# Kernel tuning notes

Measured on AMD Instinct MI355X. Metric: run time of the kernel, lower is better.

The kernel has to match this reference:

```python
import jax, jax.numpy as jnp
import numpy as np


def setup_inputs() -> dict:
    key = jax.random.key(0)
    k1, k2 = jax.random.split(key)
    x = jax.random.normal(k1, (32, 64, 64, 64), dtype=jnp.float32)  # [B, C, H, W]
    limit = 3 ** 0.5
    embeddings = jax.random.uniform(k2, (64, 512), dtype=jnp.float32,
                                    minval=-limit, maxval=limit)  # [D, K]
    return {"x": x, "embeddings": embeddings}


def reference(x, embeddings):
    B, D, H, W = x.shape
    # NCHW -> NHWC -> [N, D]
    flat_x = jnp.transpose(x, (0, 2, 3, 1)).reshape(-1, D)
    distances = (
        jnp.sum(flat_x ** 2, axis=1, keepdims=True)
        - 2.0 * flat_x @ embeddings
        + jnp.sum(embeddings ** 2, axis=0, keepdims=True)
    )
    encoding_indices = jnp.argmin(distances, axis=1)  # [N]
    # gather codebook rows: embeddings.T is [K, D]
    quantized = embeddings.T[encoding_indices].reshape(B, H, W, D)
    quantized = jnp.transpose(quantized, (0, 3, 1, 2))  # back to NCHW
    commitment_loss = jnp.mean((x - jax.lax.stop_gradient(quantized)) ** 2)
    # straight-through estimator
    quantized_ste = x + jax.lax.stop_gradient(quantized - x)
    return quantized_ste, commitment_loss, encoding_indices.reshape(B, -1)
```

## Files before the change

kernel.cpp:

```cpp
#include <hip/hip_runtime.h>

#define D      64
#define K      512
#define Q_OFF  0
#define L_OFF  8388608
#define I_OFF  8388609

#define WS_ET    0
#define WS_EN    32768
#define WS_ENH   33280
#define WS_PART  33792

#define B_LO_OFF 4096

#define SEL_SCALE 16384.0f
#define SEL_BIAS  (160.0f * 16384.0f)

typedef __attribute__((ext_vector_type(8))) short short8;
typedef __attribute__((ext_vector_type(4))) float f32x4;

static __device__ __forceinline__ unsigned short f2bf(float f) {
    unsigned u = __float_as_uint(f);
    u += 0x7fffu + ((u >> 16) & 1u);
    return (unsigned short)(u >> 16);
}
static __device__ __forceinline__ float bf2f(unsigned short h) {
    return __uint_as_float(((unsigned)h) << 16);
}

__global__ __launch_bounds__(256) void vq_prep(const float* __restrict__ E,
                                               float* __restrict__ ws,
                                               float* __restrict__ out) {
    int g = blockIdx.x * 256 + threadIdx.x;
    int t = g >> 6, lane = g & 63;
    int col = lane & 15, kg = lane >> 4;
    int code = t * 16 + col;
    short8* bhp = (short8*)out;
    short8* blp = (short8*)out + B_LO_OFF;
#pragma unroll
    for (int s = 0; s < 2; ++s) {
        short8 h, l;
#pragma unroll
        for (int j = 0; j < 8; ++j) {
            int k = s * 32 + kg * 8 + j;
            float v = -E[k * K + code];
            unsigned short hb = f2bf(v);
            h[j] = (short)hb;
            l[j] = (short)f2bf(v - bf2f(hb));
        }
        bhp[(t * 2 + s) * 64 + lane] = h;
        blp[(t * 2 + s) * 64 + lane] = l;
    }
    if (g < K) {
        float nsq = 0.f;
#pragma unroll 8
        for (int d = 0; d < D; ++d) {
            float v = E[d * K + g];
            ws[WS_ET + g * D + d] = v;
            nsq = fmaf(v, v, nsq);
        }
        ws[WS_EN + g]  = nsq;
        ws[WS_ENH + g] = 0.5f * nsq;
    }
}

__global__ __launch_bounds__(256, 2) void vq_dist(const float* __restrict__ x,
                                                  const float* __restrict__ ws,
                                                  float* __restrict__ out) {
    const int tid = threadIdx.x, w = tid >> 6, lane = tid & 63;
    const int col = lane & 15, rowg = lane >> 4;
    const int pixw = blockIdx.x * 128 + w * 32;

    short8 ah[2][2], al[2][2];
#pragma unroll
    for (int mt = 0; mt < 2; ++mt) {
        int pix = pixw + mt * 16 + col;
        const float* xp = x + ((size_t)(pix >> 12) << 18) + (pix & 4095);
#pragma unroll
        for (int s = 0; s < 2; ++s) {
            short8 h, l;
#pragma unroll
            for (int j = 0; j < 8; ++j) {
                float v = xp[(size_t)(s * 32 + rowg * 8 + j) << 12];
                unsigned short hb = f2bf(v);
                h[j] = (short)hb;
                l[j] = (short)f2bf(v - bf2f(hb));
            }
            ah[mt][s] = h; al[mt][s] = l;
        }
    }

    const short8* bhp = (const short8*)out;
    const short8* blp = (const short8*)out + B_LO_OFF;
    const float*  enh = ws + WS_ENH;

    unsigned m1[2][4], m2[2][4];
#pragma unroll
    for (int mt = 0; mt < 2; ++mt)
#pragma unroll
        for (int r = 0; r < 4; ++r) { m1[mt][r] = 0xFFFFFFFFu; m2[mt][r] = 0xFFFFFFFFu; }

    short8 pbh0[2], pbh1[2], pbl0[2], pbl1[2]; float pev[2];
    pbh0[0] = bhp[lane];        pbh1[0] = bhp[64 + lane];
    pbl0[0] = blp[lane];        pbl1[0] = blp[64 + lane];
    pev[0]  = enh[col];
    pbh0[1] = bhp[128 + lane];  pbh1[1] = bhp[192 + lane];
    pbl0[1] = blp[128 + lane];  pbl1[1] = blp[192 + lane];
    pev[1]  = enh[16 + col];

#pragma unroll 2
    for (int t = 0; t < 32; ++t) {
        const int cur = t & 1;
        const float ev = pev[cur];
        const unsigned codev = (unsigned)(t * 16 + col);

        f32x4 acc0 = { ev, ev, ev, ev };
        f32x4 acc1 = { ev, ev, ev, ev };
        acc0 = __builtin_amdgcn_mfma_f32_16x16x32_bf16(ah[0][0], pbh0[cur], acc0, 0, 0, 0);
        acc0 = __builtin_amdgcn_mfma_f32_16x16x32_bf16(al[0][0], pbh0[cur], acc0, 0, 0, 0);
        acc0 = __builtin_amdgcn_mfma_f32_16x16x32_bf16(ah[0][0], pbl0[cur], acc0, 0, 0, 0);
        acc0 = __builtin_amdgcn_mfma_f32_16x16x32_bf16(ah[0][1], pbh1[cur], acc0, 0, 0, 0);
        acc0 = __builtin_amdgcn_mfma_f32_16x16x32_bf16(al[0][1], pbh1[cur], acc0, 0, 0, 0);
        acc0 = __builtin_amdgcn_mfma_f32_16x16x32_bf16(ah[0][1], pbl1[cur], acc0, 0, 0, 0);
        acc1 = __builtin_amdgcn_mfma_f32_16x16x32_bf16(ah[1][0], pbh0[cur], acc1, 0, 0, 0);
        acc1 = __builtin_amdgcn_mfma_f32_16x16x32_bf16(al[1][0], pbh0[cur], acc1, 0, 0, 0);
        acc1 = __builtin_amdgcn_mfma_f32_16x16x32_bf16(ah[1][0], pbl0[cur], acc1, 0, 0, 0);
        acc1 = __builtin_amdgcn_mfma_f32_16x16x32_bf16(ah[1][1], pbh1[cur], acc1, 0, 0, 0);
        acc1 = __builtin_amdgcn_mfma_f32_16x16x32_bf16(al[1][1], pbh1[cur], acc1, 0, 0, 0);
        acc1 = __builtin_amdgcn_mfma_f32_16x16x32_bf16(ah[1][1], pbl1[cur], acc1, 0, 0, 0);

        if (t + 2 < 32) {
            int o = (t + 2) * 128;
            pbh0[cur] = bhp[o + lane];      pbh1[cur] = bhp[o + 64 + lane];
            pbl0[cur] = blp[o + lane];      pbl1[cur] = blp[o + 64 + lane];
            pev[cur]  = enh[(t + 2) * 16 + col];
        }

#pragma unroll
        for (int r = 0; r < 4; ++r) {
            unsigned u0 = (unsigned)fmaf(acc0[r], SEL_SCALE, SEL_BIAS);
            unsigned p0 = (u0 << 9) + codev;
            m2[0][r] = min(m2[0][r], max(m1[0][r], p0));
            m1[0][r] = min(m1[0][r], p0);
            unsigned u1 = (unsigned)fmaf(acc1[r], SEL_SCALE, SEL_BIAS);
            unsigned p1 = (u1 << 9) + codev;
            m2[1][r] = min(m2[1][r], max(m1[1][r], p1));
            m1[1][r] = min(m1[1][r], p1);
        }
    }

    unsigned* outu = (unsigned*)out;
#pragma unroll
    for (int mt = 0; mt < 2; ++mt)
#pragma unroll
        for (int r = 0; r < 4; ++r) {
            unsigned v1 = m1[mt][r], v2 = m2[mt][r];
#pragma unroll
            for (int m = 1; m < 16; m <<= 1) {
                unsigned o1 = (unsigned)__shfl_xor((int)v1, m, 16);
                unsigned o2 = (unsigned)__shfl_xor((int)v2, m, 16);
                v2 = min(max(v1, o1), min(v2, o2));
                v1 = min(v1, o1);
            }
            if (col == r) {
                int p = pixw + mt * 16 + rowg * 4 + r;
                unsigned c1 = v1 & 511u, c2 = v2 & 511u;
                outu[I_OFF + p] = c1 | (c2 << 16);
            }
        }
}

__device__ __forceinline__ float dotrow(const float* __restrict__ er,
                                        const float* __restrict__ xv) {
    const float4* e4 = (const float4*)er;
    float a0 = 0.f, a1 = 0.f, a2 = 0.f, a3 = 0.f;
#pragma unroll
    for (int q = 0; q < 16; ++q) {
        float4 e = e4[q];
        a0 = fmaf(xv[4*q+0], e.x, a0);
        a1 = fmaf(xv[4*q+1], e.y, a1);
        a2 = fmaf(xv[4*q+2], e.z, a2);
        a3 = fmaf(xv[4*q+3], e.w, a3);
    }
    return (a0 + a1) + (a2 + a3);
}

__global__ __launch_bounds__(256) void vq_out(const float* __restrict__ x,
                                              const float* __restrict__ ws,
                                              float* __restrict__ out,
                                              float* __restrict__ partial) {
    const float* ET = ws + WS_ET;
    const float* EN = ws + WS_EN;
    int n  = blockIdx.x * 256 + threadIdx.x;
    int b  = n >> 12;
    int hw = n & 4095;

    const float* xp = x + ((size_t)b << 18) + hw;
    float xv[D];
#pragma unroll
    for (int d = 0; d < D; ++d) xv[d] = xp[(size_t)d << 12];

    unsigned packed = ((const unsigned*)out)[I_OFF + n];
    int c1 = (int)(packed & 0xffffu), c2 = (int)(packed >> 16);

    float d1 = fmaf(-2.f, dotrow(ET + (c1 << 6), xv), EN[c1]);
    float d2 = fmaf(-2.f, dotrow(ET + (c2 << 6), xv), EN[c2]);
    bool sw = (d2 < d1) || (d2 == d1 && c2 < c1);
    int bestk = sw ? c2 : c1;

    out[I_OFF + n] = (float)bestk;

    const float* qv = ET + (bestk << 6);
    float* op = out + Q_OFF + ((size_t)b << 18) + hw;
    float lsum = 0.f;
#pragma unroll
    for (int d = 0; d < D; ++d) {
        float qd = qv[d];
        op[(size_t)d << 12] = qd;
        float diff = xv[d] - qd;
        lsum = fmaf(diff, diff, lsum);
    }

#pragma unroll
    for (int off = 32; off > 0; off >>= 1)
        lsum += __shfl_down(lsum, off, 64);
    __shared__ float wsum[4];
    if ((threadIdx.x & 63) == 0) wsum[threadIdx.x >> 6] = lsum;
    __syncthreads();
    if (threadIdx.x == 0)
        partial[blockIdx.x] = (wsum[0] + wsum[1]) + (wsum[2] + wsum[3]);
}

__global__ __launch_bounds__(256) void vq_final(const float* __restrict__ partial,
                                                float* __restrict__ out) {
    int t = threadIdx.x;
    float s = partial[t] + partial[t + 256];
#pragma unroll
    for (int off = 32; off > 0; off >>= 1)
        s += __shfl_down(s, off, 64);
    __shared__ float wsum[4];
    if ((t & 63) == 0) wsum[t >> 6] = s;
    __syncthreads();
    if (t == 0)
        out[L_OFF] = ((wsum[0] + wsum[1]) + (wsum[2] + wsum[3])) * (1.f / 8388608.f);
}

extern "C" void kernel_launch(void* const* d_in, const int* in_sizes, int n_in,
                              void* d_out, int out_size, void* d_ws, size_t ws_size,
                              hipStream_t stream) {
    const float* x = (const float*)d_in[0];
    const float* E = (const float*)d_in[1];
    float* out = (float*)d_out;
    float* ws  = (float*)d_ws;

    hipLaunchKernelGGL(vq_prep,  dim3(8),    dim3(256), 0, stream, E, ws, out);
    hipLaunchKernelGGL(vq_dist,  dim3(1024), dim3(256), 0, stream, x, ws, out);
    hipLaunchKernelGGL(vq_out,   dim3(512),  dim3(256), 0, stream, x, ws, out, ws + WS_PART);
    hipLaunchKernelGGL(vq_final, dim3(1),    dim3(256), 0, stream, ws + WS_PART, out);
}
```

Before: 65.82 us.

## Stage codebook tiles in LDS via async global_load_lds double buffering

```diff
diff --git a/kernel.cpp b/kernel.cpp
--- a/kernel.cpp
+++ b/kernel.cpp
@@ -26,6 +26,12 @@
 }
 static __device__ __forceinline__ float bf2f(unsigned short h) {
     return __uint_as_float(((unsigned)h) << 16);
+}
+
+__device__ __forceinline__ void gload_lds16(const float* g, float* l) {
+    __builtin_amdgcn_global_load_lds(
+        (const __attribute__((address_space(1))) unsigned int*)g,
+        (__attribute__((address_space(3))) unsigned int*)l, 16, 0, 0);
 }
 
 __global__ __launch_bounds__(256) void vq_prep(const float* __restrict__ E,
@@ -64,9 +70,11 @@
     }
 }
 
-__global__ __launch_bounds__(256, 2) void vq_dist(const float* __restrict__ x,
+__global__ __launch_bounds__(256, 4) void vq_dist(const float* __restrict__ x,
                                                   const float* __restrict__ ws,
                                                   float* __restrict__ out) {
+    __shared__ float sbuf[2][2048];
+
     const int tid = threadIdx.x, w = tid >> 6, lane = tid & 63;
     const int col = lane & 15, rowg = lane >> 4;
     const int pixw = blockIdx.x * 128 + w * 32;
@@ -90,9 +98,9 @@
         }
     }
 
-    const short8* bhp = (const short8*)out;
-    const short8* blp = (const short8*)out + B_LO_OFF;
-    const float*  enh = ws + WS_ENH;
+    const float* bh = (const float*)out;
+    const float* bl = (const float*)out + B_LO_OFF * 4;
+    const float* enh = ws + WS_ENH;
 
     unsigned m1[2][4], m2[2][4];
 #pragma unroll
@@ -100,53 +108,62 @@
 #pragma unroll
         for (int r = 0; r < 4; ++r) { m1[mt][r] = 0xFFFFFFFFu; m2[mt][r] = 0xFFFFFFFFu; }
 
-    short8 pbh0[2], pbh1[2], pbl0[2], pbl1[2]; float pev[2];
-    pbh0[0] = bhp[lane];        pbh1[0] = bhp[64 + lane];
-    pbl0[0] = blp[lane];        pbl1[0] = blp[64 + lane];
-    pev[0]  = enh[col];
-    pbh0[1] = bhp[128 + lane];  pbh1[1] = bhp[192 + lane];
-    pbl0[1] = blp[128 + lane];  pbl1[1] = blp[192 + lane];
-    pev[1]  = enh[16 + col];
-
-#pragma unroll 2
-    for (int t = 0; t < 32; ++t) {
-        const int cur = t & 1;
-        const float ev = pev[cur];
-        const unsigned codev = (unsigned)(t * 16 + col);
-
-        f32x4 acc0 = { ev, ev, ev, ev };
-        f32x4 acc1 = { ev, ev, ev, ev };
-        acc0 = __builtin_amdgcn_mfma_f32_16x16x32_bf16(ah[0][0], pbh0[cur], acc0, 0, 0, 0);
-        acc0 = __builtin_amdgcn_mfma_f32_16x16x32_bf16(al[0][0], pbh0[cur], acc0, 0, 0, 0);
-        acc0 = __builtin_amdgcn_mfma_f32_16x16x32_bf16(ah[0][0], pbl0[cur], acc0, 0, 0, 0);
-        acc0 = __builtin_amdgcn_mfma_f32_16x16x32_bf16(ah[0][1], pbh1[cur], acc0, 0, 0, 0);
-        acc0 = __builtin_amdgcn_mfma_f32_16x16x32_bf16(al[0][1], pbh1[cur], acc0, 0, 0, 0);
-        acc0 = __builtin_amdgcn_mfma_f32_16x16x32_bf16(ah[0][1], pbl1[cur], acc0, 0, 0, 0);
-        acc1 = __builtin_amdgcn_mfma_f32_16x16x32_bf16(ah[1][0], pbh0[cur], acc1, 0, 0, 0);
-        acc1 = __builtin_amdgcn_mfma_f32_16x16x32_bf16(al[1][0], pbh0[cur], acc1, 0, 0, 0);
-        acc1 = __builtin_amdgcn_mfma_f32_16x16x32_bf16(ah[1][0], pbl0[cur], acc1, 0, 0, 0);
-        acc1 = __builtin_amdgcn_mfma_f32_16x16x32_bf16(ah[1][1], pbh1[cur], acc1, 0, 0, 0);
-        acc1 = __builtin_amdgcn_mfma_f32_16x16x32_bf16(al[1][1], pbh1[cur], acc1, 0, 0, 0);
-        acc1 = __builtin_amdgcn_mfma_f32_16x16x32_bf16(ah[1][1], pbl1[cur], acc1, 0, 0, 0);
-
-        if (t + 2 < 32) {
-            int o = (t + 2) * 128;
-            pbh0[cur] = bhp[o + lane];      pbh1[cur] = bhp[o + 64 + lane];
-            pbl0[cur] = blp[o + lane];      pbl1[cur] = blp[o + 64 + lane];
-            pev[cur]  = enh[(t + 2) * 16 + col];
-        }
-
-#pragma unroll
-        for (int r = 0; r < 4; ++r) {
-            unsigned u0 = (unsigned)fmaf(acc0[r], SEL_SCALE, SEL_BIAS);
-            unsigned p0 = (u0 << 9) + codev;
-            m2[0][r] = min(m2[0][r], max(m1[0][r], p0));
-            m1[0][r] = min(m1[0][r], p0);
-            unsigned u1 = (unsigned)fmaf(acc1[r], SEL_SCALE, SEL_BIAS);
-            unsigned p1 = (u1 << 9) + codev;
-            m2[1][r] = min(m2[1][r], max(m1[1][r], p1));
-            m1[1][r] = min(m1[1][r], p1);
-        }
+    gload_lds16(bh + tid * 4, &sbuf[0][tid * 4]);
+    gload_lds16(bl + tid * 4, &sbuf[0][1024 + tid * 4]);
+    __syncthreads();
+
+    float pev = enh[col];
+
+    for (int c = 0; c < 16; ++c) {
+        if (c + 1 < 16) {
+            const float* sh = bh + (c + 1) * 1024 + tid * 4;
+            const float* sl = bl + (c + 1) * 1024 + tid * 4;
+            float* db = sbuf[(c + 1) & 1];
+            gload_lds16(sh, db + tid * 4);
+            gload_lds16(sl, db + 1024 + tid * 4);
+        }
+
+        const short8* sb = (const short8*)sbuf[c & 1];
+#pragma unroll
+        for (int p = 0; p < 2; ++p) {
+            const int t = c * 2 + p;
+            const float ev = pev;
+            pev = (t + 1 < 32) ? enh[(t + 1) * 16 + col] : 0.f;
+            const unsigned codev = (unsigned)(t * 16 + col);
+
+            short8 cbh0 = sb[p * 128 + lane];
+            short8 cbh1 = sb[p * 128 + 64 + lane];
+            short8 cbl0 = sb[256 + p * 128 + lane];
+            short8 cbl1 = sb[256 + p * 128 + 64 + lane];
+
+            f32x4 acc0 = { ev, ev, ev, ev };
+            f32x4 acc1 = { ev, ev, ev, ev };
+            acc0 = __builtin_amdgcn_mfma_f32_16x16x32_bf16(ah[0][0], cbh0, acc0, 0, 0, 0);
+            acc0 = __builtin_amdgcn_mfma_f32_16x16x32_bf16(al[0][0], cbh0, acc0, 0, 0, 0);
+            acc0 = __builtin_amdgcn_mfma_f32_16x16x32_bf16(ah[0][0], cbl0, acc0, 0, 0, 0);
+            acc0 = __builtin_amdgcn_mfma_f32_16x16x32_bf16(ah[0][1], cbh1, acc0, 0, 0, 0);
+            acc0 = __builtin_amdgcn_mfma_f32_16x16x32_bf16(al[0][1], cbh1, acc0, 0, 0, 0);
+            acc0 = __builtin_amdgcn_mfma_f32_16x16x32_bf16(ah[0][1], cbl1, acc0, 0, 0, 0);
+            acc1 = __builtin_amdgcn_mfma_f32_16x16x32_bf16(ah[1][0], cbh0, acc1, 0, 0, 0);
+            acc1 = __builtin_amdgcn_mfma_f32_16x16x32_bf16(al[1][0], cbh0, acc1, 0, 0, 0);
+            acc1 = __builtin_amdgcn_mfma_f32_16x16x32_bf16(ah[1][0], cbl0, acc1, 0, 0, 0);
+            acc1 = __builtin_amdgcn_mfma_f32_16x16x32_bf16(ah[1][1], cbh1, acc1, 0, 0, 0);
+            acc1 = __builtin_amdgcn_mfma_f32_16x16x32_bf16(al[1][1], cbh1, acc1, 0, 0, 0);
+            acc1 = __builtin_amdgcn_mfma_f32_16x16x32_bf16(ah[1][1], cbl1, acc1, 0, 0, 0);
+
+#pragma unroll
+            for (int r = 0; r < 4; ++r) {
+                unsigned u0 = (unsigned)fmaf(acc0[r], SEL_SCALE, SEL_BIAS);
+                unsigned p0 = (u0 << 9) + codev;
+                m2[0][r] = min(m2[0][r], max(m1[0][r], p0));
+                m1[0][r] = min(m1[0][r], p0);
+                unsigned u1 = (unsigned)fmaf(acc1[r], SEL_SCALE, SEL_BIAS);
+                unsigned p1 = (u1 << 9) + codev;
+                m2[1][r] = min(m2[1][r], max(m1[1][r], p1));
+                m1[1][r] = min(m1[1][r], p1);
+            }
+        }
+        __syncthreads();
     }
 
     unsigned* outu = (unsigned*)out;
```

Measured after the change: 65.18 us. About the same (-1.0%).
